# Optimization experiments

Hardware: AMD Instinct MI355X
Metric: run time of the kernel (lower is better)

Reference implementation:

```python
import jax, jax.numpy as jnp
import numpy as np

D_MODEL = 4096
N_HEADS = 32
N_KV_HEADS = 8
HEAD_DIM = D_MODEL // N_HEADS  # 128
SEQ = 2048
BATCH = 1
ROPE_BASE = 10000.0


def build_rope_cache(max_seq_len, head_dim, base=10000.0):
    half = head_dim // 2
    pos = jnp.arange(max_seq_len, dtype=jnp.float32)
    inv_freqs = 1.0 / (base ** (jnp.arange(half, dtype=jnp.float32) / half))
    angles = pos[:, None] * inv_freqs[None, :]  # (S, half)
    return jnp.cos(angles), jnp.sin(angles)


def apply_rope(t, cos, sin):
    # t: (B, H, S, D); cos/sin: (S, D//2) broadcast over batch & heads.
    t_even = t[..., 0::2]
    t_odd = t[..., 1::2]
    c = cos[None, None, :, :]
    s = sin[None, None, :, :]
    rot_even = t_even * c - t_odd * s
    rot_odd = t_even * s + t_odd * c
    # interleave back into even/odd slots
    return jnp.stack([rot_even, rot_odd], axis=-1).reshape(t.shape)


def setup_inputs() -> dict:
    key = jax.random.key(0)
    kx, kq, kk, kv, ko = jax.random.split(key, 5)
    bound = 1.0 / np.sqrt(D_MODEL)
    x = jax.random.normal(kx, (BATCH, SEQ, D_MODEL), dtype=jnp.float32)
    # torch Linear weights: (out_features, in_features)
    wq = jax.random.uniform(kq, (N_HEADS * HEAD_DIM, D_MODEL), minval=-bound, maxval=bound, dtype=jnp.float32)
    wk = jax.random.uniform(kk, (N_KV_HEADS * HEAD_DIM, D_MODEL), minval=-bound, maxval=bound, dtype=jnp.float32)
    wv = jax.random.uniform(kv, (N_KV_HEADS * HEAD_DIM, D_MODEL), minval=-bound, maxval=bound, dtype=jnp.float32)
    wo = jax.random.uniform(ko, (D_MODEL, D_MODEL), minval=-bound, maxval=bound, dtype=jnp.float32)
    attn_mask = jnp.tril(jnp.ones((SEQ, SEQ), dtype=jnp.int32))[None, None, :, :]
    return {"x": x, "wq": wq, "wk": wk, "wv": wv, "wo": wo, "attn_mask": attn_mask}


def reference(x, wq, wk, wv, wo, attn_mask):
    B, S, _ = x.shape
    cos, sin = build_rope_cache(SEQ, HEAD_DIM, ROPE_BASE)
    cos, sin = cos[:S], sin[:S]
    q = (x @ wq.T).reshape(B, S, N_HEADS, HEAD_DIM).transpose(0, 2, 1, 3)      # (B,H,S,D)
    k = (x @ wk.T).reshape(B, S, N_KV_HEADS, HEAD_DIM).transpose(0, 2, 1, 3)   # (B,Hkv,S,D)
    v = (x @ wv.T).reshape(B, S, N_KV_HEADS, HEAD_DIM).transpose(0, 2, 1, 3)
    q = apply_rope(q, cos, sin)
    k = apply_rope(k, cos, sin)
    n_rep = N_HEADS // N_KV_HEADS
    if n_rep > 1:
        k = jnp.repeat(k, n_rep, axis=1)
        v = jnp.repeat(v, n_rep, axis=1)
    scores = jnp.einsum('bhqd,bhkd->bhqk', q, k) / jnp.sqrt(jnp.float32(HEAD_DIM))
    scores = jnp.where(attn_mask == 0, -jnp.inf, scores)
    attn = jax.nn.softmax(scores, axis=-1)
    out = jnp.einsum('bhqk,bhkd->bhqd', attn, v)
    out = out.transpose(0, 2, 1, 3).reshape(B, S, D_MODEL)
    return out @ wo.T
```

## Files before the change

kernel.cpp:

```cpp
#include <hip/hip_runtime.h>
#include <hip/hip_bf16.h>

typedef float f32x2 __attribute__((ext_vector_type(2)));
typedef float f32x4 __attribute__((ext_vector_type(4)));
typedef __bf16 bf16x4 __attribute__((ext_vector_type(4)));
typedef __bf16 bf16x8 __attribute__((ext_vector_type(8)));

__device__ __forceinline__ void gld_lds16(const void* g, void* l) {
  __builtin_amdgcn_global_load_lds((const __attribute__((address_space(1))) void*)g,
                                   (__attribute__((address_space(3))) void*)l, 16, 0, 0);
}

__global__ void cvt_f32_bf16(const float* __restrict__ in, __bf16* __restrict__ out,
                             int n8) {
  int idx = blockIdx.x * blockDim.x + threadIdx.x;
  if (idx >= n8) return;
  f32x4 a = *(const f32x4*)(in + (size_t)idx * 8);
  f32x4 b = *(const f32x4*)(in + (size_t)idx * 8 + 4);
  bf16x8 o;
#pragma unroll
  for (int j = 0; j < 4; ++j) { o[j] = (__bf16)a[j]; o[4 + j] = (__bf16)b[j]; }
  *(bf16x8*)(out + (size_t)idx * 8) = o;
}

__global__ void build_trig(float* __restrict__ trig) {
  int idx = blockIdx.x * blockDim.x + threadIdx.x;
  if (idx >= 2048 * 64) return;
  int i = idx & 63, s = idx >> 6;
  float ang = (float)s * powf(10000.0f, -(float)i * (1.0f / 64.0f));
  float sn, cs;
  sincosf(ang, &sn, &cs);
  trig[idx * 2] = cs;
  trig[idx * 2 + 1] = sn;
}

template <int BM, int BN, typename OutT, bool KVF>
__global__ __launch_bounds__(256) void gemm_bf16(const __bf16* __restrict__ A,
                                                 const __bf16* __restrict__ B0,
                                                 const __bf16* __restrict__ B1,
                                                 int Nsplit, OutT* __restrict__ C,
                                                 int M, int N, int K,
                                                 const float* __restrict__ trig,
                                                 __bf16* __restrict__ Vt) {
  constexpr int MI = BM / 32, NJ = BN / 32;
  constexpr int RA = BM / 32, RB = BN / 32;
  __shared__ __bf16 As[BM * 64] __attribute__((aligned(16)));
  __shared__ __bf16 Bs[BN * 64] __attribute__((aligned(16)));

  const int tid = threadIdx.x;
  const int lane = tid & 63;
  const int w = tid >> 6;
  const int nwg = gridDim.x * gridDim.y;
  const int orig = blockIdx.y * gridDim.x + blockIdx.x;
  const int wgid = (orig & 7) * (nwg >> 3) + (orig >> 3);
  const int m0 = (wgid % gridDim.x) * BM;
  const int n0 = (wgid / gridDim.x) * BN;
  const int li = lane & 15, lg = lane >> 4;

  const __bf16* bsrc[RB];
#pragma unroll
  for (int i = 0; i < RB; ++i) {
    int slot = i * 256 + w * 64 + lane;
    int row = slot >> 3;
    int sch = (slot & 7) ^ (row & 7);
    int n = n0 + row;
    bsrc[i] = (n < Nsplit ? B0 + (size_t)n * K : B1 + (size_t)(n - Nsplit) * K) +
              sch * 8;
  }
  const __bf16* asrc[RA];
#pragma unroll
  for (int i = 0; i < RA; ++i) {
    int slot = i * 256 + w * 64 + lane;
    int row = slot >> 3;
    int sch = (slot & 7) ^ (row & 7);
    asrc[i] = A + (size_t)(m0 + row) * K + sch * 8;
  }

  const int wr = (w >> 1) * (BM / 2);
  const int wc = (w & 1) * (BN / 2);

  f32x4 acc[MI][NJ] = {};

  for (int k0 = 0; k0 < K; k0 += 64) {
    __syncthreads();
#pragma unroll
    for (int i = 0; i < RA; ++i)
      gld_lds16(asrc[i] + k0, &As[(i * 256 + w * 64) * 8]);
#pragma unroll
    for (int i = 0; i < RB; ++i)
      gld_lds16(bsrc[i] + k0, &Bs[(i * 256 + w * 64) * 8]);
    __syncthreads();

#pragma unroll
    for (int u = 0; u < 2; ++u) {
      bf16x8 af[MI], bfr[NJ];
#pragma unroll
      for (int mi = 0; mi < MI; ++mi)
        af[mi] = *(const bf16x8*)&As[(wr + mi * 16 + li) * 64 +
                                     (((u * 4 + lg) ^ (li & 7)) * 8)];
#pragma unroll
      for (int nj = 0; nj < NJ; ++nj)
        bfr[nj] = *(const bf16x8*)&Bs[(wc + nj * 16 + li) * 64 +
                                      (((u * 4 + lg) ^ (li & 7)) * 8)];
#pragma unroll
      for (int mi = 0; mi < MI; ++mi)
#pragma unroll
        for (int nj = 0; nj < NJ; ++nj)
          acc[mi][nj] = __builtin_amdgcn_mfma_f32_16x16x32_bf16(af[mi], bfr[nj],
                                                                acc[mi][nj], 0, 0, 0);
    }
  }

  const int crow = lg * 4;
  if (KVF && n0 >= Nsplit) {
#pragma unroll
    for (int mi = 0; mi < MI; ++mi)
#pragma unroll
      for (int nj = 0; nj < NJ; ++nj) {
        int d = n0 - Nsplit + wc + nj * 16 + li;
        int sb = m0 + wr + mi * 16 + crow;
        bf16x4 pk;
#pragma unroll
        for (int r = 0; r < 4; ++r) pk[r] = (__bf16)acc[mi][nj][r];
        *(bf16x4*)&Vt[(size_t)d * 2048 + sb] = pk;
      }
  } else if (KVF) {
#pragma unroll
    for (int mi = 0; mi < MI; ++mi)
#pragma unroll
      for (int nj = 0; nj < NJ; ++nj) {
        int c = n0 + wc + nj * 16 + li;
        int i = (c & 127) >> 1;
        bool even = (c & 1) == 0;
#pragma unroll
        for (int r = 0; r < 4; ++r) {
          int s = m0 + wr + mi * 16 + crow + r;
          float own = acc[mi][nj][r];
          float oth = __shfl_xor(own, 1);
          f32x2 cs = *(const f32x2*)&trig[((size_t)s * 64 + i) * 2];
          float v = even ? (own * cs[0] - oth * cs[1])
                         : (oth * cs[1] + own * cs[0]);
          C[(size_t)s * N + c] = (OutT)v;
        }
      }
  } else {
#pragma unroll
    for (int mi = 0; mi < MI; ++mi)
#pragma unroll
      for (int nj = 0; nj < NJ; ++nj)
#pragma unroll
        for (int r = 0; r < 4; ++r)
          C[(size_t)(m0 + wr + mi * 16 + crow + r) * N + (n0 + wc + nj * 16 + li)] =
              (OutT)acc[mi][nj][r];
  }
}

__global__ __launch_bounds__(256) void attn_fwd_v8(const __bf16* __restrict__ Q,
                                                   const __bf16* __restrict__ KVb,
                                                   const __bf16* __restrict__ Vt,
                                                   const float* __restrict__ trig,
                                                   __bf16* __restrict__ O) {
  const int tid = threadIdx.x;
  const int lane = tid & 63;
  const int w = tid >> 6;
  const int bid = blockIdx.x;
  const int xcd = bid & 7;
  const int r9 = bid >> 3;
  const int h = xcd * 4 + (r9 & 3);
  const int mb = 31 - (r9 >> 2);
  const int kvh = h >> 2;
  const int m0 = mb * 64;
  const int rbase = m0 + w * 16;

  __shared__ __bf16 Ks[3][32 * 128] __attribute__((aligned(16)));
  __shared__ __bf16 Vs[3][128 * 32] __attribute__((aligned(16)));
  __shared__ __bf16 Ps[4][16 * 40] __attribute__((aligned(16)));

  const int li = lane & 15, lg = lane >> 4;
  const float qscale = 0.08838834764831845f * 1.4426950408889634f;

  auto stage_k = [&](int k0, int buf) {
#pragma unroll
    for (int i = 0; i < 2; ++i) {
      int slot = i * 256 + tid;
      int row = slot >> 4;
      int sch = (slot & 15) ^ (row & 7);
      gld_lds16(&KVb[(size_t)(k0 + row) * 2048 + kvh * 128 + sch * 8],
                &Ks[buf][(i * 256 + w * 64) * 8]);
    }
  };
  auto stage_v = [&](int k0, int buf) {
#pragma unroll
    for (int i = 0; i < 2; ++i) {
      int slot = i * 256 + tid;
      int row = slot >> 2;
      int sch = (slot & 3) ^ (row & 3);
      gld_lds16(&Vt[(size_t)(kvh * 128 + row) * 2048 + k0 + sch * 8],
                &Vs[buf][(i * 256 + w * 64) * 8]);
    }
  };

  const int s = rbase + li;
  bf16x8 qf[4];
  {
    const __bf16* qrow = Q + (size_t)s * 4096 + h * 128;
#pragma unroll
    for (int kc = 0; kc < 4; ++kc) {
      bf16x8 raw = *(const bf16x8*)(qrow + kc * 32 + lg * 8);
#pragma unroll
      for (int jj = 0; jj < 4; ++jj) {
        int i = kc * 16 + lg * 4 + jj;
        f32x2 cs = *(const f32x2*)&trig[((size_t)s * 64 + i) * 2];
        float e = (float)raw[2 * jj], o = (float)raw[2 * jj + 1];
        qf[kc][2 * jj]     = (__bf16)((e * cs[0] - o * cs[1]) * qscale);
        qf[kc][2 * jj + 1] = (__bf16)((e * cs[1] + o * cs[0]) * qscale);
      }
    }
  }

  f32x4 accO[8] = {};
  float plane = 0.f;
  const int ntile = 2 * (mb + 1);

  stage_v(0, 0);
  stage_k(0, 0);

#pragma unroll 1
  for (int t = 0; t < ntile; ++t) {
    const int k0 = t * 32;
    const int cb = t % 3;
    const int nk = (t + 1 < ntile) ? k0 + 32 : k0;
    stage_v(nk, (t + 1) % 3);
    stage_k(nk, (t + 1) % 3);

    asm volatile("s_waitcnt vmcnt(4)" ::: "memory");
    __builtin_amdgcn_s_barrier();
    __builtin_amdgcn_sched_barrier(0);

    f32x4 s2[2] = {};
    __builtin_amdgcn_s_setprio(1);
#pragma unroll
    for (int nt = 0; nt < 2; ++nt)
#pragma unroll
      for (int kc = 0; kc < 4; ++kc) {
        bf16x8 kf = *(const bf16x8*)&Ks[cb][(li + 16 * nt) * 128 +
                                           (((4 * kc + lg) ^ (li & 7)) * 8)];
        s2[nt] = __builtin_amdgcn_mfma_f32_16x16x32_bf16(kf, qf[kc], s2[nt], 0, 0, 0);
      }
    __builtin_amdgcn_s_setprio(0);

    const bool needmask = (k0 + 31 > rbase);
#pragma unroll
    for (int nt = 0; nt < 2; ++nt) {
      bf16x4 pk;
#pragma unroll
      for (int rr = 0; rr < 4; ++rr) {
        const int key = k0 + 16 * nt + lg * 4 + rr;
        float v = s2[nt][rr];
        if (needmask && key > s) v = -INFINITY;
        float p = exp2f(v);
        plane += p;
        pk[rr] = (__bf16)p;
      }
      *(bf16x4*)&Ps[w][li * 40 + 16 * nt + lg * 4] = pk;
    }
    bf16x8 pa = *(const bf16x8*)&Ps[w][li * 40 + lg * 8];

    __builtin_amdgcn_s_setprio(1);
#pragma unroll
    for (int dt = 0; dt < 8; ++dt) {
      bf16x8 vf = *(const bf16x8*)&Vs[cb][(li + 16 * dt) * 32 +
                                          ((lg ^ (li & 3)) * 8)];
      accO[dt] = __builtin_amdgcn_mfma_f32_16x16x32_bf16(pa, vf, accO[dt], 0, 0, 0);
    }
    __builtin_amdgcn_s_setprio(0);
  }

  {
    float sum = plane;
    sum += __shfl_xor(sum, 16);
    sum += __shfl_xor(sum, 32);
    float inv[4];
#pragma unroll
    for (int rr = 0; rr < 4; ++rr) inv[rr] = 1.0f / __shfl(sum, lg * 4 + rr);
#pragma unroll
    for (int dt = 0; dt < 8; ++dt)
#pragma unroll
      for (int rr = 0; rr < 4; ++rr)
        O[(size_t)(rbase + lg * 4 + rr) * 4096 + h * 128 + dt * 16 + li] =
            (__bf16)(accO[dt][rr] * inv[rr]);
  }
}

extern "C" void kernel_launch(void* const* d_in, const int* in_sizes, int n_in,
                              void* d_out, int out_size, void* d_ws, size_t ws_size,
                              hipStream_t stream) {
  const float* x  = (const float*)d_in[0];
  const float* wq = (const float*)d_in[1];
  const float* wk = (const float*)d_in[2];
  const float* wv = (const float*)d_in[3];
  const float* wo = (const float*)d_in[4];
  float* out = (float*)d_out;

  const int S = 2048, D = 4096;
  char* ws = (char*)d_ws;
  __bf16* xb  = (__bf16*)ws;
  __bf16* Qb  = (__bf16*)(ws + 16777216);
  __bf16* KVb = (__bf16*)(ws + 33554432);
  __bf16* Vt  = (__bf16*)(ws + 41943040);
  __bf16* wb  = (__bf16*)(ws + 46137344);
  float*  trig = (float*)(ws + 79691776);
  __bf16* AOb = xb;

  cvt_f32_bf16<<<(S * D / 8 + 255) / 256, 256, 0, stream>>>(x, xb, S * D / 8);
  cvt_f32_bf16<<<(D * D / 8 + 255) / 256, 256, 0, stream>>>(wq, wb, D * D / 8);
  gemm_bf16<128, 128, __bf16, false><<<dim3(16, 32), 256, 0, stream>>>(
      xb, wb, wb, 1 << 30, Qb, S, D, D, nullptr, nullptr);

  build_trig<<<(2048 * 64 + 255) / 256, 256, 0, stream>>>(trig);

  cvt_f32_bf16<<<(1024 * D / 8 + 255) / 256, 256, 0, stream>>>(wk, wb, 1024 * D / 8);
  cvt_f32_bf16<<<(1024 * D / 8 + 255) / 256, 256, 0, stream>>>(wv, wb + (size_t)1024 * D,
                                                               1024 * D / 8);
  gemm_bf16<64, 128, __bf16, true><<<dim3(32, 16), 256, 0, stream>>>(
      xb, wb, wb + (size_t)1024 * D, 1024, KVb, S, 2048, D, trig, Vt);

  attn_fwd_v8<<<1024, 256, 0, stream>>>(Qb, KVb, Vt, trig, AOb);

  cvt_f32_bf16<<<(D * D / 8 + 255) / 256, 256, 0, stream>>>(wo, wb, D * D / 8);
  gemm_bf16<128, 128, float, false><<<dim3(16, 32), 256, 0, stream>>>(
      AOb, wb, wb, 1 << 30, out, S, D, D, nullptr, nullptr);
}
```

Measured before the change: 344.6 us.

## Fuse fp32 weight conversion into GEMM loads and merge Q/K/V projections

Drops the separate fp32-to-bf16 weight conversion kernels. The GEMM now streams fp32 weights directly into LDS and converts them to bf16 in registers before the MFMA. The Q, K and V projections are merged into one 6144-wide GEMM launch whose epilogue routes tiles to the Q, rotary-embedded K, or transposed V outputs. This removes several launches and the write-then-read of converted weights, but doubles B-tile LDS footprint and global read bytes per tile and adds conversion ALU work inside the main loop.

Result: slower. 457.2 us (+32.7%).

```diff
diff --git a/kernel.cpp b/kernel.cpp
--- a/kernel.cpp
+++ b/kernel.cpp
@@ -34,18 +34,18 @@
   trig[idx * 2 + 1] = sn;
 }
 
-template <int BM, int BN, typename OutT, bool KVF>
-__global__ __launch_bounds__(256) void gemm_bf16(const __bf16* __restrict__ A,
-                                                 const __bf16* __restrict__ B0,
-                                                 const __bf16* __restrict__ B1,
-                                                 int Nsplit, OutT* __restrict__ C,
-                                                 int M, int N, int K,
+template <bool QKV, typename OutT>
+__global__ __launch_bounds__(256) void gemm_f32b(const __bf16* __restrict__ A,
+                                                 const float* __restrict__ W0,
+                                                 const float* __restrict__ W1,
+                                                 const float* __restrict__ W2,
+                                                 OutT* __restrict__ C,
+                                                 __bf16* __restrict__ Kb,
+                                                 __bf16* __restrict__ Vt,
                                                  const float* __restrict__ trig,
-                                                 __bf16* __restrict__ Vt) {
-  constexpr int MI = BM / 32, NJ = BN / 32;
-  constexpr int RA = BM / 32, RB = BN / 32;
-  __shared__ __bf16 As[BM * 64] __attribute__((aligned(16)));
-  __shared__ __bf16 Bs[BN * 64] __attribute__((aligned(16)));
+                                                 int M, int N, int K) {
+  __shared__ __bf16 As[128 * 64] __attribute__((aligned(16)));
+  __shared__ float  Bsf[128 * 64] __attribute__((aligned(16)));
 
   const int tid = threadIdx.x;
   const int lane = tid & 63;
@@ -53,82 +53,93 @@
   const int nwg = gridDim.x * gridDim.y;
   const int orig = blockIdx.y * gridDim.x + blockIdx.x;
   const int wgid = (orig & 7) * (nwg >> 3) + (orig >> 3);
-  const int m0 = (wgid % gridDim.x) * BM;
-  const int n0 = (wgid / gridDim.x) * BN;
+  const int m0 = (wgid % gridDim.x) * 128;
+  const int n0 = (wgid / gridDim.x) * 128;
   const int li = lane & 15, lg = lane >> 4;
 
-  const __bf16* bsrc[RB];
-#pragma unroll
-  for (int i = 0; i < RB; ++i) {
-    int slot = i * 256 + w * 64 + lane;
-    int row = slot >> 3;
-    int sch = (slot & 7) ^ (row & 7);
-    int n = n0 + row;
-    bsrc[i] = (n < Nsplit ? B0 + (size_t)n * K : B1 + (size_t)(n - Nsplit) * K) +
-              sch * 8;
-  }
-  const __bf16* asrc[RA];
-#pragma unroll
-  for (int i = 0; i < RA; ++i) {
-    int slot = i * 256 + w * 64 + lane;
+  const __bf16* asrc[4];
+#pragma unroll
+  for (int i = 0; i < 4; ++i) {
+    int slot = i * 256 + tid;
     int row = slot >> 3;
     int sch = (slot & 7) ^ (row & 7);
     asrc[i] = A + (size_t)(m0 + row) * K + sch * 8;
   }
-
-  const int wr = (w >> 1) * (BM / 2);
-  const int wc = (w & 1) * (BN / 2);
-
-  f32x4 acc[MI][NJ] = {};
+  const float* bsrc[8];
+#pragma unroll
+  for (int i = 0; i < 8; ++i) {
+    int slot = i * 256 + tid;
+    int row = slot >> 4;
+    int gs = (slot & 15) ^ (row & 6);
+    int n = n0 + row;
+    const float* W;
+    if (QKV) W = (n < 4096) ? W0 + (size_t)n * K
+                            : (n < 5120 ? W1 + (size_t)(n - 4096) * K
+                                        : W2 + (size_t)(n - 5120) * K);
+    else     W = W0 + (size_t)n * K;
+    bsrc[i] = W + gs * 4;
+  }
+
+  const int wr = (w >> 1) * 64;
+  const int wc = (w & 1) * 64;
+
+  f32x4 acc[4][4] = {};
 
   for (int k0 = 0; k0 < K; k0 += 64) {
     __syncthreads();
 #pragma unroll
-    for (int i = 0; i < RA; ++i)
+    for (int i = 0; i < 4; ++i)
       gld_lds16(asrc[i] + k0, &As[(i * 256 + w * 64) * 8]);
 #pragma unroll
-    for (int i = 0; i < RB; ++i)
-      gld_lds16(bsrc[i] + k0, &Bs[(i * 256 + w * 64) * 8]);
+    for (int i = 0; i < 8; ++i)
+      gld_lds16(bsrc[i] + k0, &Bsf[(i * 256 + w * 64) * 4]);
     __syncthreads();
 
 #pragma unroll
     for (int u = 0; u < 2; ++u) {
-      bf16x8 af[MI], bfr[NJ];
-#pragma unroll
-      for (int mi = 0; mi < MI; ++mi)
+      bf16x8 af[4], bfr[4];
+#pragma unroll
+      for (int mi = 0; mi < 4; ++mi)
         af[mi] = *(const bf16x8*)&As[(wr + mi * 16 + li) * 64 +
                                      (((u * 4 + lg) ^ (li & 7)) * 8)];
 #pragma unroll
-      for (int nj = 0; nj < NJ; ++nj)
-        bfr[nj] = *(const bf16x8*)&Bs[(wc + nj * 16 + li) * 64 +
-                                      (((u * 4 + lg) ^ (li & 7)) * 8)];
-#pragma unroll
-      for (int mi = 0; mi < MI; ++mi)
-#pragma unroll
-        for (int nj = 0; nj < NJ; ++nj)
+      for (int nj = 0; nj < 4; ++nj) {
+        int row = wc + nj * 16 + li;
+        int s0 = (u * 8 + lg * 2) ^ (row & 6);
+        const float* bp = &Bsf[(size_t)row * 64 + s0 * 4];
+        f32x4 lo = *(const f32x4*)bp;
+        f32x4 hi = *(const f32x4*)(bp + 4);
+#pragma unroll
+        for (int j = 0; j < 4; ++j) {
+          bfr[nj][j]     = (__bf16)lo[j];
+          bfr[nj][4 + j] = (__bf16)hi[j];
+        }
+      }
+#pragma unroll
+      for (int mi = 0; mi < 4; ++mi)
+#pragma unroll
+        for (int nj = 0; nj < 4; ++nj)
           acc[mi][nj] = __builtin_amdgcn_mfma_f32_16x16x32_bf16(af[mi], bfr[nj],
                                                                 acc[mi][nj], 0, 0, 0);
     }
   }
 
   const int crow = lg * 4;
-  if (KVF && n0 >= Nsplit) {
-#pragma unroll
-    for (int mi = 0; mi < MI; ++mi)
-#pragma unroll
-      for (int nj = 0; nj < NJ; ++nj) {
-        int d = n0 - Nsplit + wc + nj * 16 + li;
-        int sb = m0 + wr + mi * 16 + crow;
-        bf16x4 pk;
-#pragma unroll
-        for (int r = 0; r < 4; ++r) pk[r] = (__bf16)acc[mi][nj][r];
-        *(bf16x4*)&Vt[(size_t)d * 2048 + sb] = pk;
-      }
-  } else if (KVF) {
-#pragma unroll
-    for (int mi = 0; mi < MI; ++mi)
-#pragma unroll
-      for (int nj = 0; nj < NJ; ++nj) {
+  if (!QKV || n0 < 4096) {
+    const int stride = QKV ? 4096 : N;
+#pragma unroll
+    for (int mi = 0; mi < 4; ++mi)
+#pragma unroll
+      for (int nj = 0; nj < 4; ++nj)
+#pragma unroll
+        for (int r = 0; r < 4; ++r)
+          C[(size_t)(m0 + wr + mi * 16 + crow + r) * stride + (n0 + wc + nj * 16 + li)] =
+              (OutT)acc[mi][nj][r];
+  } else if (n0 < 5120) {
+#pragma unroll
+    for (int mi = 0; mi < 4; ++mi)
+#pragma unroll
+      for (int nj = 0; nj < 4; ++nj) {
         int c = n0 + wc + nj * 16 + li;
         int i = (c & 127) >> 1;
         bool even = (c & 1) == 0;
@@ -140,23 +151,26 @@
           f32x2 cs = *(const f32x2*)&trig[((size_t)s * 64 + i) * 2];
           float v = even ? (own * cs[0] - oth * cs[1])
                          : (oth * cs[1] + own * cs[0]);
-          C[(size_t)s * N + c] = (OutT)v;
+          Kb[(size_t)s * 1024 + (c & 1023)] = (__bf16)v;
         }
       }
   } else {
 #pragma unroll
-    for (int mi = 0; mi < MI; ++mi)
-#pragma unroll
-      for (int nj = 0; nj < NJ; ++nj)
-#pragma unroll
-        for (int r = 0; r < 4; ++r)
-          C[(size_t)(m0 + wr + mi * 16 + crow + r) * N + (n0 + wc + nj * 16 + li)] =
-              (OutT)acc[mi][nj][r];
+    for (int mi = 0; mi < 4; ++mi)
+#pragma unroll
+      for (int nj = 0; nj < 4; ++nj) {
+        int d = (n0 + wc + nj * 16 + li) & 1023;
+        int sb = m0 + wr + mi * 16 + crow;
+        bf16x4 pk;
+#pragma unroll
+        for (int r = 0; r < 4; ++r) pk[r] = (__bf16)acc[mi][nj][r];
+        *(bf16x4*)&Vt[(size_t)d * 2048 + sb] = pk;
+      }
   }
 }
 
 __global__ __launch_bounds__(256) void attn_fwd_v8(const __bf16* __restrict__ Q,
-                                                   const __bf16* __restrict__ KVb,
+                                                   const __bf16* __restrict__ Kb,
                                                    const __bf16* __restrict__ Vt,
                                                    const float* __restrict__ trig,
                                                    __bf16* __restrict__ O) {
@@ -185,7 +199,7 @@
       int slot = i * 256 + tid;
       int row = slot >> 4;
       int sch = (slot & 15) ^ (row & 7);
-      gld_lds16(&KVb[(size_t)(k0 + row) * 2048 + kvh * 128 + sch * 8],
+      gld_lds16(&Kb[(size_t)(k0 + row) * 1024 + kvh * 128 + sch * 8],
                 &Ks[buf][(i * 256 + w * 64) * 8]);
     }
   };
@@ -306,28 +320,19 @@
   char* ws = (char*)d_ws;
   __bf16* xb  = (__bf16*)ws;
   __bf16* Qb  = (__bf16*)(ws + 16777216);
-  __bf16* KVb = (__bf16*)(ws + 33554432);
-  __bf16* Vt  = (__bf16*)(ws + 41943040);
-  __bf16* wb  = (__bf16*)(ws + 46137344);
-  float*  trig = (float*)(ws + 79691776);
+  __bf16* Kb  = (__bf16*)(ws + 33554432);
+  __bf16* Vt  = (__bf16*)(ws + 37748736);
+  float*  trig = (float*)(ws + 41943040);
   __bf16* AOb = xb;
 
   cvt_f32_bf16<<<(S * D / 8 + 255) / 256, 256, 0, stream>>>(x, xb, S * D / 8);
-  cvt_f32_bf16<<<(D * D / 8 + 255) / 256, 256, 0, stream>>>(wq, wb, D * D / 8);
-  gemm_bf16<128, 128, __bf16, false><<<dim3(16, 32), 256, 0, stream>>>(
-      xb, wb, wb, 1 << 30, Qb, S, D, D, nullptr, nullptr);
-
   build_trig<<<(2048 * 64 + 255) / 256, 256, 0, stream>>>(trig);
 
-  cvt_f32_bf16<<<(1024 * D / 8 + 255) / 256, 256, 0, stream>>>(wk, wb, 1024 * D / 8);
-  cvt_f32_bf16<<<(1024 * D / 8 + 255) / 256, 256, 0, stream>>>(wv, wb + (size_t)1024 * D,
-                                                               1024 * D / 8);
-  gemm_bf16<64, 128, __bf16, true><<<dim3(32, 16), 256, 0, stream>>>(
-      xb, wb, wb + (size_t)1024 * D, 1024, KVb, S, 2048, D, trig, Vt);
-
-  attn_fwd_v8<<<1024, 256, 0, stream>>>(Qb, KVb, Vt, trig, AOb);
-
-  cvt_f32_bf16<<<(D * D / 8 + 255) / 256, 256, 0, stream>>>(wo, wb, D * D / 8);
-  gemm_bf16<128, 128, float, false><<<dim3(16, 32), 256, 0, stream>>>(
-      AOb, wb, wb, 1 << 30, out, S, D, D, nullptr, nullptr);
-}
+  gemm_f32b<true, __bf16><<<dim3(16, 48), 256, 0, stream>>>(
+      xb, wq, wk, wv, Qb, Kb, Vt, trig, S, 6144, D);
+
+  attn_fwd_v8<<<1024, 256, 0, stream>>>(Qb, Kb, Vt, trig, AOb);
+
+  gemm_f32b<false, float><<<dim3(16, 32), 256, 0, stream>>>(
+      AOb, wo, nullptr, nullptr, out, nullptr, nullptr, nullptr, S, D, D);
+}
```
